# Kernel tuning notes

Measured on AMD Instinct MI355X. Metric: run time of the kernel, lower is better.

The kernel has to match this reference:

```python
import jax, jax.numpy as jnp
import numpy as np

N = 100_000       # nodes
E = 1_600_000     # edges (avg degree 16)
D = 64            # in_dim == out_dim
NUM_BRANCHES = 3  # branch depths 1,2,3 -> 6 GCN layers total
P_DROP = 0.5
EPS = 1e-5


def setup_inputs() -> dict:
    key = jax.random.key(0)
    k0, k1, k2 = jax.random.split(key, 3)
    x = jax.random.normal(k0, (N, D), dtype=jnp.float32)
    edge_index = jax.random.randint(k1, (2, E), 0, N, dtype=jnp.int64)
    Ws = jax.random.normal(k2, (6, D, D), dtype=jnp.float32) * (1.0 / np.sqrt(D))
    bs = jnp.zeros((6, D), dtype=jnp.float32)
    gammas = jnp.ones((6, D), dtype=jnp.float32)
    betas = jnp.zeros((6, D), dtype=jnp.float32)
    return {"x": x, "edge_index": edge_index, "Ws": Ws, "bs": bs,
            "gammas": gammas, "betas": betas}


def reference(x, edge_index, Ws, bs, gammas, betas):
    n = x.shape[0]
    loop = jnp.arange(n, dtype=edge_index.dtype)
    src = jnp.concatenate([edge_index[0], loop])  # self loops appended
    dst = jnp.concatenate([edge_index[1], loop])
    # symmetric GCN normalization D^{-1/2}(A+I)D^{-1/2}
    deg = jax.ops.segment_sum(jnp.ones_like(src, dtype=x.dtype), dst, num_segments=n)
    dis = jnp.where(deg > 0, jax.lax.rsqrt(deg), 0.0)
    norm = dis[src] * dis[dst]  # [E+N]

    def gcn_block(h, W, b, g, beta, dkey):
        # GCNConv: linear -> normalized gather/scatter aggregation -> bias
        msg = (h @ W)[src] * norm[:, None]                       # [E+N, D]
        agg = jax.ops.segment_sum(msg, dst, num_segments=n) + b  # [N, D]
        # BatchNorm1d (training mode, biased batch variance)
        mu = agg.mean(axis=0)
        var = agg.var(axis=0)
        hbn = g * (agg - mu) * jax.lax.rsqrt(var + EPS) + beta
        hr = jax.nn.relu(hbn)
        # dropout (training mode, deterministic key)
        keep = jax.random.bernoulli(dkey, 1.0 - P_DROP, hr.shape)
        return jnp.where(keep, hr / (1.0 - P_DROP), 0.0)

    dkeys = jax.random.split(jax.random.key(42), 6)
    outs = [x]
    idx = 0
    for bi in range(NUM_BRANCHES):
        h = x
        for _ in range(bi + 1):
            h = gcn_block(h, Ws[idx], bs[idx], gammas[idx], betas[idx], dkeys[idx])
            idx += 1
        outs.append(h)
    return jnp.concatenate(outs, axis=1)  # [N, in_dim + 3*out_dim] = [N, 256]
```

## Files before the change

kernel.cpp:

```cpp
#include <hip/hip_runtime.h>
#include <stdint.h>

__host__ __device__ static inline void threefry2x32(uint32_t k0, uint32_t k1,
                                                    uint32_t x0, uint32_t x1,
                                                    uint32_t* o0, uint32_t* o1) {
  uint32_t ks2 = k0 ^ k1 ^ 0x1BD11BDAu;
  x0 += k0; x1 += k1;
#define TF_RND(r) { x0 += x1; x1 = (x1 << (r)) | (x1 >> (32 - (r))); x1 ^= x0; }
  TF_RND(13) TF_RND(15) TF_RND(26) TF_RND(6)
  x0 += k1; x1 += ks2 + 1u;
  TF_RND(17) TF_RND(29) TF_RND(16) TF_RND(24)
  x0 += ks2; x1 += k0 + 2u;
  TF_RND(13) TF_RND(15) TF_RND(26) TF_RND(6)
  x0 += k0; x1 += k1 + 3u;
  TF_RND(17) TF_RND(29) TF_RND(16) TF_RND(24)
  x0 += k1; x1 += ks2 + 4u;
  TF_RND(13) TF_RND(15) TF_RND(26) TF_RND(6)
  x0 += ks2; x1 += k0 + 5u;
#undef TF_RND
  *o0 = x0; *o1 = x1;
}

__global__ void k_detect(const int* __restrict__ ei, int twoE, int* __restrict__ flag) {
  int lane = threadIdx.x & 63;
  int v = (2 * lane + 1 < twoE) ? ei[2 * lane + 1] : 0;
  unsigned long long nz = __ballot(v != 0);
  if (lane == 0) flag[0] = (nz == 0ull) ? 1 : 0;
}

__device__ static inline int load_idx(const void* p, long long i, int is64) {
  return is64 ? (int)((const long long*)p)[i] : ((const int*)p)[i];
}

__global__ void k_hist(const void* __restrict__ ei, int E, int* __restrict__ cnt,
                       const int* __restrict__ flag) {
  int is64 = flag[0];
  for (int e = blockIdx.x * blockDim.x + threadIdx.x; e < E; e += gridDim.x * blockDim.x) {
    int d = load_idx(ei, (long long)E + e, is64);
    atomicAdd(&cnt[d], 1);
  }
}

__global__ __launch_bounds__(1024) void k_scan(const int* __restrict__ cnt,
                                               int* __restrict__ rp,
                                               float* __restrict__ dis, int n) {
  __shared__ int sd[1024];
  int tid = threadIdx.x;
  int chunk = (n + 1023) >> 10;
  int start = tid * chunk;
  int end = min(start + chunk, n);
  int s = 0;
  for (int i = start; i < end; ++i) s += cnt[i];
  sd[tid] = s;
  __syncthreads();
  for (int off = 1; off < 1024; off <<= 1) {
    int v = (tid >= off) ? sd[tid - off] : 0;
    __syncthreads();
    sd[tid] += v;
    __syncthreads();
  }
  int run = (tid == 0) ? 0 : sd[tid - 1];
  for (int i = start; i < end; ++i) {
    int c = cnt[i];
    rp[i] = run;
    dis[i] = rsqrtf((float)c + 1.0f);
    run += c;
  }
  if (tid == 1023) rp[n] = sd[1023];
}

__global__ void k_place(const void* __restrict__ ei, int E, const int* __restrict__ rp,
                        int* __restrict__ cursor, int* __restrict__ colA,
                        const int* __restrict__ flag) {
  int is64 = flag[0];
  for (int e = blockIdx.x * blockDim.x + threadIdx.x; e < E; e += gridDim.x * blockDim.x) {
    int s = load_idx(ei, e, is64);
    int d = load_idx(ei, (long long)E + e, is64);
    int pos = rp[d] + atomicAdd(&cursor[d], 1);
    colA[pos] = s;
  }
}

__global__ void k_copyx(const float4* __restrict__ x4, float4* __restrict__ out4, int n) {
  int total = n * 16;
  for (int i = blockIdx.x * blockDim.x + threadIdx.x; i < total; i += gridDim.x * blockDim.x) {
    int r = i >> 4, c = i & 15;
    out4[(size_t)r * 64 + c] = x4[i];
  }
}

__global__ __launch_bounds__(256) void k_gemm(const float* __restrict__ H,
                                              const float* __restrict__ W,
                                              const float* __restrict__ dis,
                                              float* __restrict__ Yp, int n) {
  __shared__ float Wl[64 * 64];
  int tid = threadIdx.x;
  {
    const float4* Wv = (const float4*)W;
    float4* Wlv = (float4*)Wl;
#pragma unroll
    for (int i = 0; i < 4; ++i) Wlv[tid + i * 256] = Wv[tid + i * 256];
  }
  __syncthreads();
  int row = blockIdx.x * 64 + (tid >> 2);
  if (row >= n) return;
  int tx = tid & 3;
  const float4* h4 = (const float4*)(H + (size_t)row * 64);
  float acc[16];
#pragma unroll
  for (int c = 0; c < 16; ++c) acc[c] = 0.0f;
#pragma unroll
  for (int k4 = 0; k4 < 16; ++k4) {
    float4 a = h4[k4];
    const float* w0 = &Wl[(k4 * 4 + 0) * 64 + tx * 16];
    const float* w1 = &Wl[(k4 * 4 + 1) * 64 + tx * 16];
    const float* w2 = &Wl[(k4 * 4 + 2) * 64 + tx * 16];
    const float* w3 = &Wl[(k4 * 4 + 3) * 64 + tx * 16];
#pragma unroll
    for (int c = 0; c < 16; ++c) {
      acc[c] = fmaf(a.x, w0[c], acc[c]);
      acc[c] = fmaf(a.y, w1[c], acc[c]);
      acc[c] = fmaf(a.z, w2[c], acc[c]);
      acc[c] = fmaf(a.w, w3[c], acc[c]);
    }
  }
  float dv = dis[row];
  float4* o = (float4*)(Yp + (size_t)row * 64 + tx * 16);
#pragma unroll
  for (int q = 0; q < 4; ++q) {
    float4 v;
    v.x = acc[q * 4 + 0] * dv;
    v.y = acc[q * 4 + 1] * dv;
    v.z = acc[q * 4 + 2] * dv;
    v.w = acc[q * 4 + 3] * dv;
    o[q] = v;
  }
}

__global__ __launch_bounds__(256) void k_agg(const float* __restrict__ Yp,
                                             const int* __restrict__ rp,
                                             const int* __restrict__ colA,
                                             const float* __restrict__ dis,
                                             const float* __restrict__ bias,
                                             float* __restrict__ AGG,
                                             double* __restrict__ stats, int n) {
  __shared__ double red[512];
  int tid = threadIdx.x;
  int lane = tid & 63;
  int gw = (blockIdx.x * blockDim.x + tid) >> 6;
  int nw = (gridDim.x * blockDim.x) >> 6;
  double s0 = 0.0, s1 = 0.0;
  float b = bias[lane];
  for (int v = gw; v < n; v += nw) {
    float a0 = Yp[(size_t)v * 64 + lane];
    float a1 = 0.f, a2 = 0.f, a3 = 0.f, a4 = 0.f, a5 = 0.f, a6 = 0.f, a7 = 0.f;
    int beg = rp[v], end = rp[v + 1];
    for (int j0 = beg; j0 < end; j0 += 64) {
      int nn = min(64, end - j0);
      int c = (lane < nn) ? colA[j0 + lane] : 0;
      int t = 0;
      for (; t + 8 <= nn; t += 8) {
        int i0 = __shfl(c, t);
        int i1 = __shfl(c, t + 1);
        int i2 = __shfl(c, t + 2);
        int i3 = __shfl(c, t + 3);
        int i4 = __shfl(c, t + 4);
        int i5 = __shfl(c, t + 5);
        int i6 = __shfl(c, t + 6);
        int i7 = __shfl(c, t + 7);
        a0 += Yp[(size_t)i0 * 64 + lane];
        a1 += Yp[(size_t)i1 * 64 + lane];
        a2 += Yp[(size_t)i2 * 64 + lane];
        a3 += Yp[(size_t)i3 * 64 + lane];
        a4 += Yp[(size_t)i4 * 64 + lane];
        a5 += Yp[(size_t)i5 * 64 + lane];
        a6 += Yp[(size_t)i6 * 64 + lane];
        a7 += Yp[(size_t)i7 * 64 + lane];
      }
      for (; t + 4 <= nn; t += 4) {
        int i0 = __shfl(c, t);
        int i1 = __shfl(c, t + 1);
        int i2 = __shfl(c, t + 2);
        int i3 = __shfl(c, t + 3);
        a0 += Yp[(size_t)i0 * 64 + lane];
        a1 += Yp[(size_t)i1 * 64 + lane];
        a2 += Yp[(size_t)i2 * 64 + lane];
        a3 += Yp[(size_t)i3 * 64 + lane];
      }
      for (; t < nn; ++t) {
        int i0 = __shfl(c, t);
        a0 += Yp[(size_t)i0 * 64 + lane];
      }
    }
    float val = fmaf(dis[v], ((a0 + a1) + (a2 + a3)) + ((a4 + a5) + (a6 + a7)), b);
    AGG[(size_t)v * 64 + lane] = val;
    s0 += (double)val;
    s1 += (double)val * (double)val;
  }
  red[tid] = s0;
  red[256 + tid] = s1;
  __syncthreads();
  if (tid < 64) {
    double t0 = red[tid] + red[64 + tid] + red[128 + tid] + red[192 + tid];
    double t1 = red[256 + tid] + red[320 + tid] + red[384 + tid] + red[448 + tid];
    atomicAdd(&stats[tid], t0);
    atomicAdd(&stats[64 + tid], t1);
  }
}

__global__ __launch_bounds__(256) void k_bn(const float* __restrict__ AGG,
                                            const double* __restrict__ stats,
                                            const float* __restrict__ g,
                                            const float* __restrict__ beta,
                                            float* __restrict__ dst, int ldo,
                                            uint32_t k0, uint32_t k1, int n,
                                            double invn) {
  __shared__ float ssc[64], ssh[64];
  if (threadIdx.x < 64) {
    int c = threadIdx.x;
    double mu = stats[c] * invn;
    double var = stats[64 + c] * invn - mu * mu;
    double scale = (double)g[c] / sqrt(var + 1e-5);
    ssc[c] = (float)scale;
    ssh[c] = (float)((double)beta[c] - mu * scale);
  }
  __syncthreads();
  int total = n * 64;
  for (int j = blockIdx.x * blockDim.x + threadIdx.x; j < total; j += gridDim.x * blockDim.x) {
    uint32_t b0, b1;
    threefry2x32(k0, k1, 0u, (uint32_t)j, &b0, &b1);
    uint32_t bits = b0 ^ b1;
    int col = j & 63;
    int row = j >> 6;
    float sc = ssc[col], sh = ssh[col];
    float v1 = AGG[j];
    float o1 = (bits & 0x80000000u) ? 0.0f : fmaxf(fmaf(sc, v1, sh), 0.0f) * 2.0f;
    dst[(size_t)row * ldo + col] = o1;
  }
}

extern "C" void kernel_launch(void* const* d_in, const int* in_sizes, int n_in,
                              void* d_out, int out_size, void* d_ws, size_t ws_size,
                              hipStream_t stream) {
  const float* x = (const float*)d_in[0];
  const void* ei = d_in[1];
  const float* Ws = (const float*)d_in[2];
  const float* bs = (const float*)d_in[3];
  const float* gs = (const float*)d_in[4];
  const float* betas = (const float*)d_in[5];
  float* out = (float*)d_out;

  int N = in_sizes[0] / 64;
  int E = in_sizes[1] / 2;

  size_t off = 0;
  auto alloc = [&](size_t bytes) -> void* {
    void* p = (char*)d_ws + off;
    off += (bytes + 255) & ~(size_t)255;
    return p;
  };
  float* Yp   = (float*)alloc((size_t)N * 64 * 4);
  float* AGG  = (float*)alloc((size_t)N * 64 * 4);
  float* Hb   = (float*)alloc((size_t)N * 64 * 4);
  int* rp     = (int*)alloc(((size_t)N + 1) * 4);
  int* colA   = (int*)alloc((size_t)E * 4);
  int* cnt    = (int*)alloc((size_t)N * 4);
  int* cursor = (int*)alloc((size_t)N * 4);
  float* dis  = (float*)alloc((size_t)N * 4);
  double* stats = (double*)alloc(6 * 128 * 8);
  int* flag   = (int*)alloc(256);

  uint32_t dk0[6], dk1[6];
  for (int i = 0; i < 6; ++i)
    threefry2x32(0u, 42u, 0u, (uint32_t)i, &dk0[i], &dk1[i]);

  hipMemsetAsync(cnt, 0, (size_t)N * 4, stream);
  hipMemsetAsync(cursor, 0, (size_t)N * 4, stream);
  hipMemsetAsync(stats, 0, 6 * 128 * 8, stream);

  k_detect<<<1, 64, 0, stream>>>((const int*)ei, 2 * E, flag);
  k_hist<<<2048, 256, 0, stream>>>(ei, E, cnt, flag);
  k_scan<<<1, 1024, 0, stream>>>(cnt, rp, dis, N);
  k_place<<<2048, 256, 0, stream>>>(ei, E, rp, cursor, colA, flag);
  k_copyx<<<2048, 256, 0, stream>>>((const float4*)x, (float4*)out, N);

  int gemm_blocks = (N + 63) / 64;
  int idx = 0;
  for (int bi = 0; bi < 3; ++bi) {
    const float* hin = x;
    for (int li = 0; li <= bi; ++li, ++idx) {
      k_gemm<<<gemm_blocks, 256, 0, stream>>>(hin, Ws + (size_t)idx * 4096, dis, Yp, N);
      k_agg<<<1024, 256, 0, stream>>>(Yp, rp, colA, dis, bs + idx * 64, AGG,
                                      stats + idx * 128, N);
      bool last = (li == bi);
      float* dst = last ? (out + 64 * (bi + 1)) : Hb;
      int ldo = last ? 256 : 64;
      k_bn<<<2048, 256, 0, stream>>>(AGG, stats + idx * 128, gs + idx * 64,
                                     betas + idx * 64, dst, ldo, dk0[idx], dk1[idx],
                                     N, 1.0 / (double)N);
      hin = Hb;
    }
  }
}
```

Before: 1.264 ms.

## Replace single-block CSR prefix scan with multi-block three-pass scan; double agg grid

The serial single-block scan over node degree counts, where each of 1024 threads walks about 98 elements in a strided pattern, is replaced by a three-kernel scan. Per-block partial sums are computed, a single block scans the roughly 391 partials, and each block then writes its row pointers and inverse-sqrt degrees in parallel. This targets the latency of a one-workgroup kernel with uncoalesced sequential loops, at the cost of two extra kernel launches. Separately, the aggregation kernel grid is doubled from 1024 to 2048 blocks. The new scan relies on the block count staying at or below 512.

```diff
diff --git a/kernel.cpp b/kernel.cpp
--- a/kernel.cpp
+++ b/kernel.cpp
@@ -41,32 +41,57 @@
   }
 }
 
-__global__ __launch_bounds__(1024) void k_scan(const int* __restrict__ cnt,
+__global__ __launch_bounds__(256) void k_part(const int* __restrict__ cnt,
+                                              int* __restrict__ partial, int n) {
+  __shared__ int red[256];
+  int tid = threadIdx.x;
+  int i = blockIdx.x * 256 + tid;
+  red[tid] = (i < n) ? cnt[i] : 0;
+  __syncthreads();
+  for (int off = 128; off > 0; off >>= 1) {
+    if (tid < off) red[tid] += red[tid + off];
+    __syncthreads();
+  }
+  if (tid == 0) partial[blockIdx.x] = red[0];
+}
+
+__global__ __launch_bounds__(512) void k_scanp(const int* __restrict__ partial,
+                                               int* __restrict__ poff,
+                                               int* __restrict__ rp, int nblk, int n) {
+  __shared__ int sd[512];
+  int tid = threadIdx.x;
+  sd[tid] = (tid < nblk) ? partial[tid] : 0;
+  __syncthreads();
+  for (int off = 1; off < 512; off <<= 1) {
+    int v = (tid >= off) ? sd[tid - off] : 0;
+    __syncthreads();
+    sd[tid] += v;
+    __syncthreads();
+  }
+  if (tid < nblk) poff[tid] = (tid == 0) ? 0 : sd[tid - 1];
+  if (tid == 511) rp[n] = sd[511];
+}
+
+__global__ __launch_bounds__(256) void k_write(const int* __restrict__ cnt,
+                                               const int* __restrict__ poff,
                                                int* __restrict__ rp,
                                                float* __restrict__ dis, int n) {
-  __shared__ int sd[1024];
-  int tid = threadIdx.x;
-  int chunk = (n + 1023) >> 10;
-  int start = tid * chunk;
-  int end = min(start + chunk, n);
-  int s = 0;
-  for (int i = start; i < end; ++i) s += cnt[i];
-  sd[tid] = s;
-  __syncthreads();
-  for (int off = 1; off < 1024; off <<= 1) {
+  __shared__ int sd[256];
+  int tid = threadIdx.x;
+  int i = blockIdx.x * 256 + tid;
+  int c = (i < n) ? cnt[i] : 0;
+  sd[tid] = c;
+  __syncthreads();
+  for (int off = 1; off < 256; off <<= 1) {
     int v = (tid >= off) ? sd[tid - off] : 0;
     __syncthreads();
     sd[tid] += v;
     __syncthreads();
   }
-  int run = (tid == 0) ? 0 : sd[tid - 1];
-  for (int i = start; i < end; ++i) {
-    int c = cnt[i];
-    rp[i] = run;
+  if (i < n) {
+    rp[i] = poff[blockIdx.x] + sd[tid] - c;
     dis[i] = rsqrtf((float)c + 1.0f);
-    run += c;
-  }
-  if (tid == 1023) rp[n] = sd[1023];
+  }
 }
 
 __global__ void k_place(const void* __restrict__ ei, int E, const int* __restrict__ rp,
@@ -252,6 +277,7 @@
 
   int N = in_sizes[0] / 64;
   int E = in_sizes[1] / 2;
+  int nblk = (N + 255) / 256;
 
   size_t off = 0;
   auto alloc = [&](size_t bytes) -> void* {
@@ -268,6 +294,8 @@
   int* cursor = (int*)alloc((size_t)N * 4);
   float* dis  = (float*)alloc((size_t)N * 4);
   double* stats = (double*)alloc(6 * 128 * 8);
+  int* partial = (int*)alloc((size_t)nblk * 4);
+  int* poff    = (int*)alloc((size_t)nblk * 4);
   int* flag   = (int*)alloc(256);
 
   uint32_t dk0[6], dk1[6];
@@ -280,7 +308,9 @@
 
   k_detect<<<1, 64, 0, stream>>>((const int*)ei, 2 * E, flag);
   k_hist<<<2048, 256, 0, stream>>>(ei, E, cnt, flag);
-  k_scan<<<1, 1024, 0, stream>>>(cnt, rp, dis, N);
+  k_part<<<nblk, 256, 0, stream>>>(cnt, partial, N);
+  k_scanp<<<1, 512, 0, stream>>>(partial, poff, rp, nblk, N);
+  k_write<<<nblk, 256, 0, stream>>>(cnt, poff, rp, dis, N);
   k_place<<<2048, 256, 0, stream>>>(ei, E, rp, cursor, colA, flag);
   k_copyx<<<2048, 256, 0, stream>>>((const float4*)x, (float4*)out, N);
 
@@ -290,7 +320,7 @@
     const float* hin = x;
     for (int li = 0; li <= bi; ++li, ++idx) {
       k_gemm<<<gemm_blocks, 256, 0, stream>>>(hin, Ws + (size_t)idx * 4096, dis, Yp, N);
-      k_agg<<<1024, 256, 0, stream>>>(Yp, rp, colA, dis, bs + idx * 64, AGG,
+      k_agg<<<2048, 256, 0, stream>>>(Yp, rp, colA, dis, bs + idx * 64, AGG,
                                       stats + idx * 128, N);
       bool last = (li == bi);
       float* dst = last ? (out + 64 * (bi + 1)) : Hb;
```

Result: faster. 1.131 ms (-10.5%).
